# Kernel tuning notes

Measured on AMD Instinct MI355X. Metric: run time of the kernel, lower is better.

The kernel has to match this reference:

```python
import jax, jax.numpy as jnp
import numpy as np

B, S, C, M, L = 32, 8192, 64, 16, 4  # batch, seq, n_enc, n_modes, n_layers


def setup_inputs() -> dict:
    key = jax.random.key(0)
    ks = jax.random.split(key, 12)
    scale = 1.0 / (C * M)
    return {
        "input_tensor": jax.random.normal(ks[0], (B, S, 1), dtype=jnp.float32),
        "enc_w": jax.random.normal(ks[1], (C, 1), dtype=jnp.float32) * 0.1,
        "enc_b": jax.random.normal(ks[2], (C,), dtype=jnp.float32) * 0.1,
        "R_re": jax.random.normal(ks[3], (L, C, C, M), dtype=jnp.float32) * scale,
        "R_im": jax.random.normal(ks[4], (L, C, C, M), dtype=jnp.float32) * scale,
        "Wl_w": jax.random.normal(ks[5], (L, C, C), dtype=jnp.float32) * 0.1,
        "Wl_b": jax.random.normal(ks[6], (L, C), dtype=jnp.float32) * 0.1,
        "d1_w": jax.random.normal(ks[7], (C, C), dtype=jnp.float32) * 0.1,
        "d1_b": jax.random.normal(ks[8], (C,), dtype=jnp.float32) * 0.1,
        "d2_w": jax.random.normal(ks[9], (1, C), dtype=jnp.float32) * 0.1,
        "d2_b": jax.random.normal(ks[10], (1,), dtype=jnp.float32) * 0.1,
    }


def reference(input_tensor, enc_w, enc_b, R_re, R_im, Wl_w, Wl_b, d1_w, d1_b, d2_w, d2_b):
    # encoder: Conv1d(1, C, k=1) == per-position dense over channel dim
    h = jnp.einsum('bsi,ci->bsc', input_tensor, enc_w) + enc_b  # [B,S,C]
    n_freq = S // 2 + 1
    for l in range(L):
        x_cs = jnp.swapaxes(h, 1, 2)                 # [B,C,S]
        x_ft = jnp.fft.rfft(x_cs, axis=-1)           # [B,C,n_freq] complex
        Rl = R_re[l] + 1j * R_im[l]                  # [C,C,M]
        y = jnp.einsum('bim,iom->bom', x_ft[:, :, :M], Rl)  # [B,C,M]
        y_full = jnp.concatenate(
            [y, jnp.zeros((B, C, n_freq - M), dtype=y.dtype)], axis=-1)
        spat = jnp.fft.irfft(y_full, n=S, axis=-1)   # [B,C,S] float32
        wout = jnp.einsum('oi,bis->bos', Wl_w[l], x_cs) + Wl_b[l][None, :, None]
        h = jax.nn.gelu(jnp.swapaxes(spat + wout, 1, 2), approximate=False)
    z = jax.nn.gelu(jnp.einsum('bsc,oc->bso', h, d1_w) + d1_b, approximate=False)
    out = jnp.einsum('bso,po->bsp', z, d2_w) + d2_b  # [B,S,1]
    return out
```

## Files before the change

### kernel.cpp

```cpp
#include <hip/hip_runtime.h>
#include <math.h>

#define NB 32
#define NS 8192
#define NC 64
#define NM 16
#define NL 4
#define NM2 32
#define TPOS 128
#define NT (NS/TPOS)

typedef float f16v __attribute__((ext_vector_type(16)));
typedef float f8v  __attribute__((ext_vector_type(8)));

static __device__ __forceinline__ f8v zero8() {
    f8v v;
    #pragma unroll
    for (int j = 0; j < 8; ++j) v[j] = 0.0f;
    return v;
}

static __device__ __forceinline__ float gelu_fast(float v) {
    float x  = v * 0.7071067811865475f;
    float ax = fabsf(x);
    float d  = fmaf(0.3275911f, ax, 1.0f);
    float t;
    asm("v_rcp_f32 %0, %1" : "=v"(t) : "v"(d));
    float p = t * fmaf(t, fmaf(t, fmaf(t, fmaf(t, 1.061405429f, -1.453152027f),
                                       1.421413741f), -0.284496736f),
                       0.254829592f);
    float e = __expf(-ax * ax);
    float erfv = fmaf(-p, e, 1.0f);
    erfv = copysignf(erfv, x);
    return 0.5f * v * (1.0f + erfv);
}

__global__ void k_table(float* __restrict__ T) {
    int s = blockIdx.x * blockDim.x + threadIdx.x;
    if (s >= NS) return;
    const float w = 6.283185307179586f / (float)NS;
    float* row = T + (size_t)s * NM2;
    #pragma unroll
    for (int m = 0; m < NM; ++m) {
        int idx = (m * s) & (NS - 1);
        float a = w * (float)idx;
        float sv, cv;
        sincosf(a, &sv, &cv);
        row[2*m]   = cv;
        row[2*m+1] = sv;
    }
}

__global__ void k_prep(const float* __restrict__ Ww, const float* __restrict__ d1w,
                       float* __restrict__ Wt, float* __restrict__ d1t) {
    int idx = blockIdx.x * 256 + threadIdx.x;
    if (idx < NL*NC*NC) {
        int l = idx / (NC*NC), r = idx % (NC*NC);
        int i = r / NC, o = r % NC;
        Wt[idx] = Ww[(size_t)l*NC*NC + (size_t)o*NC + i];
    } else if (idx < NL*NC*NC + NC*NC) {
        int r = idx - NL*NC*NC;
        int i = r / NC, o = r % NC;
        d1t[r] = d1w[(size_t)o*NC + i];
    }
}

static __device__ __forceinline__ void dft_phase(
        const float* __restrict__ hs, const float* __restrict__ T,
        float* __restrict__ partial, int b, int tile, int s0,
        int og, int t) {
    int c = t & 63;
    int cm = c & 31;
    const float* hrow = hs + c * TPOS;
    f8v acc = zero8();
    const float* trow = T + (size_t)s0 * NM2 + og * 8;
    #pragma unroll 4
    for (int ss = 0; ss < TPOS; ++ss) {
        float hv = hrow[ss ^ cm];
        f8v tv = *(const f8v*)(trow + (size_t)ss * NM2);
        acc += hv * tv;
    }
    float* pout = partial + (((size_t)b*NT + tile)*NC + c)*NM2 + og*8;
    *(f8v*)pout = acc;
}

__global__ void __launch_bounds__(256) k_enc(const float* __restrict__ x,
                                             const float* __restrict__ ew,
                                             const float* __restrict__ eb,
                                             const float* __restrict__ T,
                                             float* __restrict__ h,
                                             float* __restrict__ partial) {
    __shared__ float hs[NC * TPOS];
    int tile = blockIdx.x, b = blockIdx.y;
    int t = threadIdx.x;
    int og = __builtin_amdgcn_readfirstlane(t >> 6);
    int p  = t & 63;
    int s0 = tile * TPOS;

    float xA = x[(size_t)b*NS + s0 + p];
    float xB = x[(size_t)b*NS + s0 + p + 64];
    f16v ew16 = *(const f16v*)(ew + og*16);
    f16v eb16 = *(const f16v*)(eb + og*16);
    f16v hA = xA * ew16 + eb16;
    f16v hB = xB * ew16 + eb16;

    *(f16v*)(h + ((size_t)b*NS + s0 + p)*NC + og*16)      = hA;
    *(f16v*)(h + ((size_t)b*NS + s0 + p + 64)*NC + og*16) = hB;

    #pragma unroll
    for (int j = 0; j < 16; ++j) {
        int c = og*16 + j;
        int off = p ^ (c & 31);
        hs[c*TPOS + off]      = hA[j];
        hs[c*TPOS + off + 64] = hB[j];
    }
    __syncthreads();

    dft_phase(hs, T, partial, b, tile, s0, og, t);
}

__global__ void __launch_bounds__(256) k_mix(const float* __restrict__ partial,
                                             const float* __restrict__ Rre,
                                             const float* __restrict__ Rim,
                                             float* __restrict__ yst, int l) {
    __shared__ float xf[NC * 8];
    int b = blockIdx.x, jg = blockIdx.y, t = threadIdx.x;
    #pragma unroll
    for (int e = 0; e < 2; ++e) {
        int idx = t + 256*e;
        int c = idx >> 3, kk = idx & 7;
        const float* pp = partial + (size_t)b*NT*NC*NM2 + (size_t)c*NM2 + 8*jg + kk;
        float s = 0.f;
        #pragma unroll 8
        for (int tile = 0; tile < NT; ++tile)
            s += pp[(size_t)tile * NC * NM2];
        xf[idx] = s;
    }
    __syncthreads();
    {
        int o = t >> 2, mq = t & 3;
        int m = 4*jg + mq;
        float yre = 0.f, yim = 0.f;
        #pragma unroll 8
        for (int i = 0; i < NC; ++i) {
            float xr = xf[i*8 + 2*mq];
            float xs = xf[i*8 + 2*mq + 1];
            size_t ridx = (((size_t)l*NC + i)*NC + o)*NM + m;
            float rr = Rre[ridx], ri = Rim[ridx];
            yre = fmaf(xr, rr, yre); yre = fmaf(xs, ri, yre);
            yim = fmaf(xr, ri, yim); yim = fmaf(-xs, rr, yim);
        }
        float* yb = yst + (size_t)b*NM2*NC;
        if (m == 0) { yb[o] = yre * (1.0f/NS); yb[NC + o] = 0.f; }
        else {
            yb[(size_t)(2*m)*NC + o]   = yre * (2.0f/NS);
            yb[(size_t)(2*m+1)*NC + o] = -yim * (2.0f/NS);
        }
    }
}

template<bool LAST>
__global__ void __launch_bounds__(256) k_spec(float* __restrict__ h,
                                              const float* __restrict__ T,
                                              const float* __restrict__ yst,
                                              const float* __restrict__ Wt,
                                              const float* __restrict__ Wb,
                                              const float* __restrict__ d1t,
                                              const float* __restrict__ d1b,
                                              const float* __restrict__ d2w,
                                              const float* __restrict__ d2b,
                                              float* __restrict__ partial,
                                              float* __restrict__ outp,
                                              int l) {
    __shared__ float hs[NC * TPOS];
    int tile = blockIdx.x, b = blockIdx.y;
    int t = threadIdx.x;
    int og = __builtin_amdgcn_readfirstlane(t >> 6);
    int p  = t & 63;
    int s0 = tile * TPOS;

    const float4* hblk = (const float4*)(h + ((size_t)b*NS + s0)*NC);
    float4 ld0 = hblk[t];
    float4 ld1 = hblk[t + 256];
    float4 ld2 = hblk[t + 512];
    float4 ld3 = hblk[t + 768];
    float4 ld4 = hblk[t + 1024];
    float4 ld5 = hblk[t + 1280];
    float4 ld6 = hblk[t + 1536];
    float4 ld7 = hblk[t + 1792];

    const float* Wl = Wt + (size_t)l*NC*NC + og*16;
    const float* bl = Wb + (size_t)l*NC + og*16;
    const float* yb = yst + (size_t)b*NM2*NC + og*16;

    f16v accA = *(const f16v*)bl;
    f16v accB = accA;

    {
        f16v y0 = *(const f16v*)yb;
        accA += y0;
        accB += y0;
        float rev = (float)(s0 + p) * (1.0f / (float)NS);
        float cA1, sA1;
        asm("v_cos_f32 %0, %1" : "=v"(cA1) : "v"(rev));
        asm("v_sin_f32 %0, %1" : "=v"(sA1) : "v"(rev));
        const float cd = 0.99879545620517239f;
        const float sd = 0.04906767432741802f;
        float cB1 = cA1*cd - sA1*sd;
        float sB1 = sA1*cd + cA1*sd;
        float cmA = cA1, smA = sA1, cmB = cB1, smB = sB1;
        #pragma unroll 1
        for (int m = 1; m < NM; ++m) {
            f16v yc  = *(const f16v*)(yb + (size_t)(2*m)*NC);
            f16v ysv = *(const f16v*)(yb + (size_t)(2*m+1)*NC);
            accA += cmA * yc;  accA += smA * ysv;
            accB += cmB * yc;  accB += smB * ysv;
            float cnA = cmA*cA1 - smA*sA1;
            smA = cmA*sA1 + smA*cA1;  cmA = cnA;
            float cnB = cmB*cB1 - smB*sB1;
            smB = cmB*sB1 + smB*cB1;  cmB = cnB;
        }
    }

    {
        float4 lds[8] = {ld0, ld1, ld2, ld3, ld4, ld5, ld6, ld7};
        #pragma unroll
        for (int jj = 0; jj < 8; ++jj) {
            int idx = t + 256*jj;
            int pos = idx >> 4;
            int cbase = (idx & 15) * 4;
            float vals[4] = {lds[jj].x, lds[jj].y, lds[jj].z, lds[jj].w};
            #pragma unroll
            for (int j2 = 0; j2 < 4; ++j2) {
                int c = cbase + j2;
                hs[c*TPOS + (pos ^ (c & 31))] = vals[j2];
            }
        }
    }
    __syncthreads();

    #pragma unroll 8
    for (int i = 0; i < NC; ++i) {
        int off = p ^ (i & 31);
        float va = hs[i*TPOS + off];
        float vb = hs[i*TPOS + off + 64];
        f16v w = *(const f16v*)(Wl + (size_t)i*NC);
        accA += va * w;
        accB += vb * w;
    }

    f16v gA, gB;
    #pragma unroll
    for (int j = 0; j < 16; ++j) gA[j] = gelu_fast(accA[j]);
    #pragma unroll
    for (int j = 0; j < 16; ++j) gB[j] = gelu_fast(accB[j]);
    if (!LAST) {
        *(f16v*)(h + ((size_t)b*NS + s0 + p)*NC + og*16)      = gA;
        *(f16v*)(h + ((size_t)b*NS + s0 + p + 64)*NC + og*16) = gB;
    }

    __syncthreads();
    #pragma unroll
    for (int j = 0; j < 16; ++j) {
        int c = og*16 + j;
        int off = p ^ (c & 31);
        hs[c*TPOS + off]      = gA[j];
        hs[c*TPOS + off + 64] = gB[j];
    }
    __syncthreads();

    if (!LAST) {
        dft_phase(hs, T, partial, b, tile, s0, og, t);
    } else {
        f16v aA = *(const f16v*)(d1b + og*16);
        f16v aB = aA;
        #pragma unroll 8
        for (int i = 0; i < NC; ++i) {
            int off = p ^ (i & 31);
            float va = hs[i*TPOS + off];
            float vb = hs[i*TPOS + off + 64];
            f16v w = *(const f16v*)(d1t + (size_t)i*NC + og*16);
            aA += va * w;
            aB += vb * w;
        }
        float resA = 0.f, resB = 0.f;
        #pragma unroll
        for (int j = 0; j < 16; ++j) {
            float dw = d2w[og*16 + j];
            resA = fmaf(gelu_fast(aA[j]), dw, resA);
            resB = fmaf(gelu_fast(aB[j]), dw, resB);
        }
        __syncthreads();
        hs[og*TPOS + p]      = resA;
        hs[og*TPOS + p + 64] = resB;
        __syncthreads();
        if (t < TPOS) {
            outp[(size_t)b*NS + s0 + t] = d2b[0] + hs[t] + hs[TPOS + t]
                                        + hs[2*TPOS + t] + hs[3*TPOS + t];
        }
    }
}

extern "C" void kernel_launch(void* const* d_in, const int* in_sizes, int n_in,
                              void* d_out, int out_size, void* d_ws, size_t ws_size,
                              hipStream_t stream) {
    const float* input = (const float*)d_in[0];
    const float* enc_w = (const float*)d_in[1];
    const float* enc_b = (const float*)d_in[2];
    const float* R_re  = (const float*)d_in[3];
    const float* R_im  = (const float*)d_in[4];
    const float* Wl_w  = (const float*)d_in[5];
    const float* Wl_b  = (const float*)d_in[6];
    const float* d1_w  = (const float*)d_in[7];
    const float* d1_b  = (const float*)d_in[8];
    const float* d2_w  = (const float*)d_in[9];
    const float* d2_b  = (const float*)d_in[10];
    float* out = (float*)d_out;

    float* ws  = (float*)d_ws;
    float* h   = ws;
    float* T   = h   + (size_t)NB*NS*NC;
    float* par = T   + (size_t)NS*NM2;
    float* yst = par + (size_t)NB*NT*NC*NM2;
    float* Wt  = yst + (size_t)NB*NM2*NC;
    float* d1t = Wt  + (size_t)NL*NC*NC;

    hipLaunchKernelGGL(k_table, dim3(NS/256), dim3(256), 0, stream, T);
    hipLaunchKernelGGL(k_prep, dim3((NL*NC*NC + NC*NC + 255)/256), dim3(256), 0,
                       stream, Wl_w, d1_w, Wt, d1t);
    hipLaunchKernelGGL(k_enc, dim3(NT, NB), dim3(256), 0, stream,
                       input, enc_w, enc_b, T, h, par);
    for (int l = 0; l < NL; ++l) {
        hipLaunchKernelGGL(k_mix, dim3(NB, 4), dim3(256), 0, stream,
                           par, R_re, R_im, yst, l);
        if (l < NL - 1) {
            hipLaunchKernelGGL((k_spec<false>), dim3(NT, NB), dim3(256), 0, stream,
                               h, T, yst, Wt, Wl_b, d1t, d1_b, d2_w, d2_b,
                               par, out, l);
        } else {
            hipLaunchKernelGGL((k_spec<true>), dim3(NT, NB), dim3(256), 0, stream,
                               h, T, yst, Wt, Wl_b, d1t, d1_b, d2_w, d2_b,
                               par, out, l);
        }
    }
}
```

Before: 386.2 us.

## Switch shared tile to position-major padded layout with vectorized LDS access

The shared-memory tile moves from a channel-major, XOR-swizzled layout to a position-major layout with a row stride of 65 floats. Global loads and activation results can now be written to LDS with float4 stores, and the channel-mixing and decoder matmuls read four channels per float4 load instead of issuing scalar swizzled reads. The DFT phase reads with a padded stride so that lanes indexed by channel avoid bank conflicts. The odd stride of 65 means many float4 addresses are not 16-byte aligned, so those vector LDS accesses may be split or hit bank conflicts. They also depend on unaligned-LDS support being present.

```diff
diff --git a/kernel.cpp b/kernel.cpp
--- a/kernel.cpp
+++ b/kernel.cpp
@@ -9,6 +9,7 @@
 #define NM2 32
 #define TPOS 128
 #define NT (NS/TPOS)
+#define PAD 65
 
 typedef float f16v __attribute__((ext_vector_type(16)));
 typedef float f8v  __attribute__((ext_vector_type(8)));
@@ -70,13 +71,11 @@
         float* __restrict__ partial, int b, int tile, int s0,
         int og, int t) {
     int c = t & 63;
-    int cm = c & 31;
-    const float* hrow = hs + c * TPOS;
     f8v acc = zero8();
     const float* trow = T + (size_t)s0 * NM2 + og * 8;
     #pragma unroll 4
     for (int ss = 0; ss < TPOS; ++ss) {
-        float hv = hrow[ss ^ cm];
+        float hv = hs[ss * PAD + c];
         f8v tv = *(const f8v*)(trow + (size_t)ss * NM2);
         acc += hv * tv;
     }
@@ -90,7 +89,7 @@
                                              const float* __restrict__ T,
                                              float* __restrict__ h,
                                              float* __restrict__ partial) {
-    __shared__ float hs[NC * TPOS];
+    __shared__ float hs[TPOS * PAD];
     int tile = blockIdx.x, b = blockIdx.y;
     int t = threadIdx.x;
     int og = __builtin_amdgcn_readfirstlane(t >> 6);
@@ -107,12 +106,12 @@
     *(f16v*)(h + ((size_t)b*NS + s0 + p)*NC + og*16)      = hA;
     *(f16v*)(h + ((size_t)b*NS + s0 + p + 64)*NC + og*16) = hB;
 
-    #pragma unroll
-    for (int j = 0; j < 16; ++j) {
-        int c = og*16 + j;
-        int off = p ^ (c & 31);
-        hs[c*TPOS + off]      = hA[j];
-        hs[c*TPOS + off + 64] = hB[j];
+    float4* dA = (float4*)&hs[p*PAD + og*16];
+    float4* dB = (float4*)&hs[(p+64)*PAD + og*16];
+    #pragma unroll
+    for (int q = 0; q < 4; ++q) {
+        dA[q] = make_float4(hA[4*q], hA[4*q+1], hA[4*q+2], hA[4*q+3]);
+        dB[q] = make_float4(hB[4*q], hB[4*q+1], hB[4*q+2], hB[4*q+3]);
     }
     __syncthreads();
 
@@ -172,7 +171,7 @@
                                               float* __restrict__ partial,
                                               float* __restrict__ outp,
                                               int l) {
-    __shared__ float hs[NC * TPOS];
+    __shared__ float hs[TPOS * PAD];
     int tile = blockIdx.x, b = blockIdx.y;
     int t = threadIdx.x;
     int og = __builtin_amdgcn_readfirstlane(t >> 6);
@@ -223,30 +222,32 @@
     }
 
     {
-        float4 lds[8] = {ld0, ld1, ld2, ld3, ld4, ld5, ld6, ld7};
-        #pragma unroll
-        for (int jj = 0; jj < 8; ++jj) {
-            int idx = t + 256*jj;
-            int pos = idx >> 4;
-            int cbase = (idx & 15) * 4;
-            float vals[4] = {lds[jj].x, lds[jj].y, lds[jj].z, lds[jj].w};
-            #pragma unroll
-            for (int j2 = 0; j2 < 4; ++j2) {
-                int c = cbase + j2;
-                hs[c*TPOS + (pos ^ (c & 31))] = vals[j2];
-            }
-        }
-    }
-    __syncthreads();
-
-    #pragma unroll 8
-    for (int i = 0; i < NC; ++i) {
-        int off = p ^ (i & 31);
-        float va = hs[i*TPOS + off];
-        float vb = hs[i*TPOS + off + 64];
-        f16v w = *(const f16v*)(Wl + (size_t)i*NC);
-        accA += va * w;
-        accB += vb * w;
+        int ss = t >> 4, q4 = (t & 15) * 4;
+        *(float4*)&hs[ss*PAD + q4]       = ld0;
+        *(float4*)&hs[(ss+16)*PAD + q4]  = ld1;
+        *(float4*)&hs[(ss+32)*PAD + q4]  = ld2;
+        *(float4*)&hs[(ss+48)*PAD + q4]  = ld3;
+        *(float4*)&hs[(ss+64)*PAD + q4]  = ld4;
+        *(float4*)&hs[(ss+80)*PAD + q4]  = ld5;
+        *(float4*)&hs[(ss+96)*PAD + q4]  = ld6;
+        *(float4*)&hs[(ss+112)*PAD + q4] = ld7;
+    }
+    __syncthreads();
+
+    const float* hA = &hs[p * PAD];
+    const float* hB = &hs[(p + 64) * PAD];
+    #pragma unroll 4
+    for (int i4 = 0; i4 < NC; i4 += 4) {
+        float4 va = *(const float4*)(hA + i4);
+        float4 vb = *(const float4*)(hB + i4);
+        f16v w0 = *(const f16v*)(Wl + (size_t)i4*NC);
+        f16v w1 = *(const f16v*)(Wl + (size_t)(i4+1)*NC);
+        f16v w2 = *(const f16v*)(Wl + (size_t)(i4+2)*NC);
+        f16v w3 = *(const f16v*)(Wl + (size_t)(i4+3)*NC);
+        accA += va.x * w0;  accB += vb.x * w0;
+        accA += va.y * w1;  accB += vb.y * w1;
+        accA += va.z * w2;  accB += vb.z * w2;
+        accA += va.w * w3;  accB += vb.w * w3;
     }
 
     f16v gA, gB;
@@ -260,12 +261,14 @@
     }
 
     __syncthreads();
-    #pragma unroll
-    for (int j = 0; j < 16; ++j) {
-        int c = og*16 + j;
-        int off = p ^ (c & 31);
-        hs[c*TPOS + off]      = gA[j];
-        hs[c*TPOS + off + 64] = gB[j];
+    {
+        float4* dA = (float4*)&hs[p*PAD + og*16];
+        float4* dB = (float4*)&hs[(p+64)*PAD + og*16];
+        #pragma unroll
+        for (int q = 0; q < 4; ++q) {
+            dA[q] = make_float4(gA[4*q], gA[4*q+1], gA[4*q+2], gA[4*q+3]);
+            dB[q] = make_float4(gB[4*q], gB[4*q+1], gB[4*q+2], gB[4*q+3]);
+        }
     }
     __syncthreads();
 
@@ -274,14 +277,20 @@
     } else {
         f16v aA = *(const f16v*)(d1b + og*16);
         f16v aB = aA;
-        #pragma unroll 8
-        for (int i = 0; i < NC; ++i) {
-            int off = p ^ (i & 31);
-            float va = hs[i*TPOS + off];
-            float vb = hs[i*TPOS + off + 64];
-            f16v w = *(const f16v*)(d1t + (size_t)i*NC + og*16);
-            aA += va * w;
-            aB += vb * w;
+        const float* hA2 = &hs[p * PAD];
+        const float* hB2 = &hs[(p + 64) * PAD];
+        #pragma unroll 4
+        for (int i4 = 0; i4 < NC; i4 += 4) {
+            float4 va = *(const float4*)(hA2 + i4);
+            float4 vb = *(const float4*)(hB2 + i4);
+            f16v w0 = *(const f16v*)(d1t + (size_t)i4*NC + og*16);
+            f16v w1 = *(const f16v*)(d1t + (size_t)(i4+1)*NC + og*16);
+            f16v w2 = *(const f16v*)(d1t + (size_t)(i4+2)*NC + og*16);
+            f16v w3 = *(const f16v*)(d1t + (size_t)(i4+3)*NC + og*16);
+            aA += va.x * w0;  aB += vb.x * w0;
+            aA += va.y * w1;  aB += vb.y * w1;
+            aA += va.z * w2;  aB += vb.z * w2;
+            aA += va.w * w3;  aB += vb.w * w3;
         }
         float resA = 0.f, resB = 0.f;
         #pragma unroll
```

Result: slower. 413.4 us (+7.0%).
